# Kernel optimization log

Measured on AMD Instinct MI355X. Metric: run time of the kernel, lower is better.

Reference implementation:

```python
import jax, jax.numpy as jnp
import numpy as np

TOPK = 4


def setup_inputs() -> dict:
    key = jax.random.key(0)
    ks = jax.random.split(key, 9)
    B, T, D = 4, 2048, 1024
    E, H = 32, 128          # routed experts, per-expert hidden
    HS = H * TOPK           # shared expert hidden = 512
    s = lambda k, shape, fan: jax.random.normal(k, shape, dtype=jnp.float32) / np.sqrt(fan)
    return {
        "x": jax.random.normal(ks[0], (B, T, D), dtype=jnp.float32),
        "router_w": s(ks[1], (E, D), D),
        "router_bias": jnp.zeros((E,), dtype=jnp.float32),
        "gate_w": s(ks[2], (E, H, D), D),
        "up_w": s(ks[3], (E, H, D), D),
        "down_w": s(ks[4], (E, D, H), H),
        "sgate_w": s(ks[5], (HS, D), D),
        "sup_w": s(ks[6], (HS, D), D),
        "sdown_w": s(ks[7], (D, HS), HS),
    }


def reference(x, router_w, router_bias, gate_w, up_w, down_w, sgate_w, sup_w, sdown_w):
    B, T, D = x.shape
    flat = x.reshape(B * T, D)                                   # [N, D]
    # Router (fp32 logits + persistent bias buffer)
    logits = flat.astype(jnp.float32) @ router_w.T + router_bias  # [N, E]
    scores = jax.nn.softmax(logits, axis=-1)
    topk_scores, topk_idx = jax.lax.top_k(scores, TOPK)          # [N, K]
    topk_scores = topk_scores / jnp.clip(
        topk_scores.sum(axis=-1, keepdims=True), 1e-12, None)
    # Dense all-expert SwiGLU (matches torch.stack over experts)
    h = jax.nn.silu(jnp.einsum("nd,ehd->neh", flat, gate_w)) \
        * jnp.einsum("nd,ehd->neh", flat, up_w)                  # [N, E, H]
    expert_out = jnp.einsum("neh,edh->ned", h, down_w)           # [N, E, D]
    # Gather top-k expert outputs, scale, combine
    sel = jnp.take_along_axis(expert_out, topk_idx[:, :, None], axis=1)  # [N, K, D]
    out = (sel * topk_scores.astype(flat.dtype)[:, :, None]).sum(axis=1)  # [N, D]
    # Always-on shared expert (SwiGLU)
    out = out + (jax.nn.silu(flat @ sgate_w.T) * (flat @ sup_w.T)) @ sdown_w.T
    return out.reshape(B, T, D)
```

## Files before the change

### kernel.cpp

```cpp
#include <hip/hip_runtime.h>
#include <hip/hip_bf16.h>
#include <math.h>

#define N_TOK 8192
#define DIM   1024
#define E_R   32
#define H_E   128
#define HS    512
#define TOPK  4
#define RKS   8
#define RKL   (DIM / RKS)
#define MAXSLOT 34816

typedef __bf16 bf16;
typedef __bf16 bf16x8 __attribute__((ext_vector_type(8)));
typedef float  floatx4 __attribute__((ext_vector_type(4)));

#define MFMA16(a,b,c) __builtin_amdgcn_mfma_f32_16x16x32_bf16(a,b,c,0,0,0)

__device__ __forceinline__ void gl_lds16(const bf16* g, bf16* l) {
    __builtin_amdgcn_global_load_lds(
        (const __attribute__((address_space(1))) void*)g,
        (__attribute__((address_space(3))) void*)l, 16, 0, 0);
}

__global__ __launch_bounds__(256)
void cvt_all(const float* __restrict__ x, const float* __restrict__ g,
             const float* __restrict__ u, const float* __restrict__ d,
             const float* __restrict__ sg, const float* __restrict__ su,
             const float* __restrict__ sd,
             bf16* __restrict__ xb, bf16* __restrict__ gb, bf16* __restrict__ ub,
             bf16* __restrict__ db, bf16* __restrict__ sgb, bf16* __restrict__ sub,
             bf16* __restrict__ sdb) {
    int b = blockIdx.x;
    const float* s; bf16* o; int lb;
    if      (b < 4096)  { s = x;  o = xb;  lb = b; }
    else if (b < 6144)  { s = g;  o = gb;  lb = b - 4096; }
    else if (b < 8192)  { s = u;  o = ub;  lb = b - 6144; }
    else if (b < 10240) { s = d;  o = db;  lb = b - 8192; }
    else if (b < 10496) { s = sg; o = sgb; lb = b - 10240; }
    else if (b < 10752) { s = su; o = sub; lb = b - 10496; }
    else                { s = sd; o = sdb; lb = b - 10752; }
    size_t i = (size_t)lb * 2048 + threadIdx.x * 8;
    float4 v0 = *(const float4*)(s + i);
    float4 v1 = *(const float4*)(s + i + 4);
    bf16x8 r = {(bf16)v0.x,(bf16)v0.y,(bf16)v0.z,(bf16)v0.w,
                (bf16)v1.x,(bf16)v1.y,(bf16)v1.z,(bf16)v1.w};
    *(bf16x8*)(o + i) = r;
}

__global__ __launch_bounds__(256)
void router_gemm(const float* __restrict__ x, const float* __restrict__ rw,
                 float* __restrict__ partial) {
    __shared__ float Xs[64 * 132];
    __shared__ float Wt[128 * 32];
    int tid = threadIdx.x;
    int t0  = blockIdx.x * 64;
    int kb  = blockIdx.y * RKL;

#pragma unroll
    for (int j = 0; j < 8; ++j) {
        int flat = j * 1024 + tid * 4;
        int row = flat >> 7, col = flat & 127;
        float4 v = *(const float4*)(x + (size_t)(t0 + row) * DIM + kb + col);
        *(float4*)(&Xs[row * 132 + col]) = v;
    }
    {
        int e = tid >> 3, kq = (tid & 7) * 16;
        const float* wp = rw + (size_t)e * DIM + kb + kq;
#pragma unroll
        for (int i = 0; i < 16; i += 4) {
            float4 v = *(const float4*)(wp + i);
            Wt[(kq + i + 0) * 32 + e] = v.x;
            Wt[(kq + i + 1) * 32 + e] = v.y;
            Wt[(kq + i + 2) * 32 + e] = v.z;
            Wt[(kq + i + 3) * 32 + e] = v.w;
        }
    }
    __syncthreads();

    int eg = tid & 7, tg = tid >> 3;
    float acc[2][4] = {{0.f}};
#pragma unroll 4
    for (int k = 0; k < RKL; k += 4) {
        float4 xa0 = *(const float4*)(&Xs[(tg * 2 + 0) * 132 + k]);
        float4 xa1 = *(const float4*)(&Xs[(tg * 2 + 1) * 132 + k]);
#pragma unroll
        for (int kk = 0; kk < 4; ++kk) {
            float4 w = *(const float4*)(&Wt[(k + kk) * 32 + eg * 4]);
            float x0 = (&xa0.x)[kk], x1 = (&xa1.x)[kk];
            acc[0][0] += x0 * w.x; acc[0][1] += x0 * w.y;
            acc[0][2] += x0 * w.z; acc[0][3] += x0 * w.w;
            acc[1][0] += x1 * w.x; acc[1][1] += x1 * w.y;
            acc[1][2] += x1 * w.z; acc[1][3] += x1 * w.w;
        }
    }
#pragma unroll
    for (int t = 0; t < 2; ++t) {
        floatx4 v = { acc[t][0], acc[t][1], acc[t][2], acc[t][3] };
        *(floatx4*)(&partial[((size_t)blockIdx.y * N_TOK + t0 + tg * 2 + t) * 32 + eg * 4]) = v;
    }
}

__global__ __launch_bounds__(256)
void router_fin(const float* __restrict__ partial, const float* __restrict__ rb,
                int* __restrict__ counts, int* __restrict__ tlist,
                float* __restrict__ slist, int* __restrict__ tok2slot) {
    __shared__ int lcnt[E_R];
    __shared__ int gbase[E_R];
    int tid = threadIdx.x;
    int n = blockIdx.x * 256 + tid;
    if (tid < E_R) lcnt[tid] = 0;
    __syncthreads();

    float lg[E_R];
#pragma unroll
    for (int e4 = 0; e4 < E_R; e4 += 4) {
        floatx4 s = {0.f, 0.f, 0.f, 0.f};
#pragma unroll
        for (int ks = 0; ks < RKS; ++ks)
            s += *(const floatx4*)(&partial[((size_t)ks * N_TOK + n) * 32 + e4]);
        lg[e4 + 0] = s[0] + rb[e4 + 0];
        lg[e4 + 1] = s[1] + rb[e4 + 1];
        lg[e4 + 2] = s[2] + rb[e4 + 2];
        lg[e4 + 3] = s[3] + rb[e4 + 3];
    }
    float mx = -1e30f;
#pragma unroll
    for (int e = 0; e < E_R; ++e) mx = fmaxf(mx, lg[e]);
    float se = 0.f;
#pragma unroll
    for (int e = 0; e < E_R; ++e) { float v = __expf(lg[e] - mx); lg[e] = v; se += v; }
    float inv = 1.f / se;

    unsigned usedMask = 0;
    int idx[TOPK]; float pv[TOPK]; int lpos[TOPK]; float psum = 0.f;
    for (int k = 0; k < TOPK; ++k) {
        float best = -1.f; int bi = 0;
        for (int e = 0; e < E_R; ++e)
            if (!((usedMask >> e) & 1) && lg[e] > best) { best = lg[e]; bi = e; }
        usedMask |= 1u << bi;
        idx[k] = bi; pv[k] = best * inv; psum += pv[k];
    }
    float norm = 1.f / fmaxf(psum, 1e-12f);
#pragma unroll
    for (int k = 0; k < TOPK; ++k)
        lpos[k] = atomicAdd(&lcnt[idx[k]], 1);
    __syncthreads();
    if (tid < E_R) gbase[tid] = atomicAdd(&counts[tid], lcnt[tid]);
    __syncthreads();
#pragma unroll
    for (int k = 0; k < TOPK; ++k) {
        int e = idx[k];
        int pos = gbase[e] + lpos[k];
        tlist[(size_t)e * N_TOK + pos] = n;
        slist[(size_t)e * N_TOK + pos] = pv[k] * norm;
        tok2slot[(size_t)n * 4 + k] = (e << 16) | pos;
    }
}

__global__ void wq_build(const int* __restrict__ counts, int* __restrict__ items,
                         int* __restrict__ nitems, int* __restrict__ expbase) {
    if (threadIdx.x == 0) {
        int n = 0, base = 0;
        for (int e = 0; e < E_R; ++e) {
            int c = counts[e];
            expbase[e] = base;
            int nt = (c + 63) >> 6;
            for (int t = 0; t < nt; ++t)
                items[n++] = (e << 24) | (t << 16) | (base + t * 64);
            base += nt * 64;
        }
        *nitems = n;
    }
}

__global__ __launch_bounds__(256, 3)
void phase1(const bf16* __restrict__ xb, const bf16* __restrict__ wg,
            const bf16* __restrict__ wu, const bf16* __restrict__ sg,
            const bf16* __restrict__ su, const int* __restrict__ counts,
            const int* __restrict__ tlist, const int* __restrict__ items,
            const int* __restrict__ nitems,
            bf16* __restrict__ Hg, bf16* __restrict__ Hs) {
    __shared__ __align__(16) bf16 As[2 * 64 * 32];
    __shared__ __align__(16) bf16 Bs[2 * 256 * 32];

    int b = blockIdx.x;
    const bf16 *gptr, *uptr;
    bf16* hout; int hstride;
    int e, lbase, cnt = 0;
    if (b < 512) {
        int c = b >> 7, t = b & 127;
        gptr = sg + (size_t)c * H_E * DIM;
        uptr = su + (size_t)c * H_E * DIM;
        hout = Hs + (size_t)t * 64 * HS + c * H_E;
        hstride = HS;
        lbase = t * 64;
        e = -1;
    } else {
        int rbk = b - 512;
        if (rbk >= *nitems) return;
        int it = items[rbk];
        e = it >> 24; int t = (it >> 16) & 0xff; int rowbase = it & 0xffff;
        gptr = wg + (size_t)e * H_E * DIM;
        uptr = wu + (size_t)e * H_E * DIM;
        hout = Hg + (size_t)rowbase * H_E;
        hstride = H_E;
        cnt = counts[e];
        lbase = t * 64;
    }

    int tid = threadIdx.x;
    int r = tid >> 2;
    int chunk = (tid & 3) * 8;
    int tok;
    if (e < 0) tok = lbase + r;
    else { int li = lbase + r; if (li >= cnt) li = cnt - 1; tok = tlist[(size_t)e * N_TOK + li]; }
    const bf16* aSrc = xb + (size_t)tok * DIM + chunk;
    const bf16* gSrc = gptr + (size_t)r * DIM + chunk;
    const bf16* uSrc = uptr + (size_t)r * DIM + chunk;

    int w = tid >> 6, lane = tid & 63, m = lane & 15, quad = lane >> 4;

    floatx4 aG[4][2] = {{{0}}};
    floatx4 aU[4][2] = {{{0}}};

    #define P1_STAGE(buf, k0)                                                  \
        do {                                                                   \
            bf16* aD = As + (buf) * 2048 + tid * 8;                            \
            bf16* bD = Bs + (buf) * 8192 + tid * 8;                            \
            gl_lds16(aSrc + (k0), aD);                                         \
            gl_lds16(gSrc + (k0), bD);                                         \
            gl_lds16(gSrc + 64 * DIM + (k0), bD + 2048);                       \
            gl_lds16(uSrc + (k0), bD + 4096);                                  \
            gl_lds16(uSrc + 64 * DIM + (k0), bD + 6144);                       \
        } while (0)

    P1_STAGE(0, 0);
    __syncthreads();

    int cur = 0;
    for (int k0 = 0; k0 < DIM; k0 += 32) {
        if (k0 + 32 < DIM) P1_STAGE(cur ^ 1, k0 + 32);
        const bf16* Ab = As + cur * 2048;
        const bf16* Bb = Bs + cur * 8192;
        bf16x8 a[4], bg[2], bu[2];
#pragma unroll
        for (int mg = 0; mg < 4; ++mg)
            a[mg] = *(const bf16x8*)(Ab + (mg * 16 + m) * 32 + quad * 8);
#pragma unroll
        for (int j = 0; j < 2; ++j) {
            bg[j] = *(const bf16x8*)(Bb + (w * 32 + j * 16 + m) * 32 + quad * 8);
            bu[j] = *(const bf16x8*)(Bb + (128 + w * 32 + j * 16 + m) * 32 + quad * 8);
        }
#pragma unroll
        for (int j = 0; j < 2; ++j)
#pragma unroll
            for (int mg = 0; mg < 4; ++mg) {
                aG[mg][j] = MFMA16(a[mg], bg[j], aG[mg][j]);
                aU[mg][j] = MFMA16(a[mg], bu[j], aU[mg][j]);
            }
        __syncthreads();
        cur ^= 1;
    }
    #undef P1_STAGE

#pragma unroll
    for (int mg = 0; mg < 4; ++mg)
#pragma unroll
        for (int j = 0; j < 2; ++j)
#pragma unroll
            for (int r4 = 0; r4 < 4; ++r4) {
                float gv = aG[mg][j][r4], uv = aU[mg][j][r4];
                float h = gv / (1.f + __expf(-gv)) * uv;
                hout[(size_t)(mg * 16 + quad * 4 + r4) * hstride + w * 32 + j * 16 + m] = (bf16)h;
            }
}

__global__ __launch_bounds__(256, 3)
void phase2(const bf16* __restrict__ Hg, const bf16* __restrict__ wd,
            const int* __restrict__ counts, const float* __restrict__ slist,
            const int* __restrict__ items, const int* __restrict__ nitems,
            bf16* __restrict__ Od) {
    __shared__ __align__(16) bf16 As[2 * 64 * 32];
    __shared__ __align__(16) bf16 Bs[2 * 256 * 32];
    __shared__ float ssc[64];

    int rbk = blockIdx.x;
    if (rbk >= *nitems) return;
    int it = items[rbk];
    int e = it >> 24, t = (it >> 16) & 0xff, rowbase = it & 0xffff;
    int n0 = blockIdx.y * 256;
    int cnt = counts[e];

    int tid = threadIdx.x;
    if (tid < 64) {
        int li = t * 64 + tid;
        ssc[tid] = (li < cnt) ? slist[(size_t)e * N_TOK + li] : 0.f;
    }

    int r = tid >> 2, chunk = (tid & 3) * 8;
    const bf16* aSrc = Hg + (size_t)(rowbase + r) * H_E + chunk;
    const bf16* bSrc = wd + (size_t)e * DIM * H_E + (size_t)(n0 + r) * H_E + chunk;

    int w = tid >> 6, lane = tid & 63, m = lane & 15, quad = lane >> 4;
    floatx4 acc[4][4] = {{{0}}};

    #define P2_STAGE(buf, k0)                                                  \
        do {                                                                   \
            bf16* aD = As + (buf) * 2048 + tid * 8;                            \
            bf16* bD = Bs + (buf) * 8192 + tid * 8;                            \
            gl_lds16(aSrc + (k0), aD);                                         \
            _Pragma("unroll")                                                  \
            for (int p = 0; p < 4; ++p)                                        \
                gl_lds16(bSrc + (size_t)p * 64 * H_E + (k0), bD + p * 2048);   \
        } while (0)

    P2_STAGE(0, 0);
    __syncthreads();

    int cur = 0;
    for (int k0 = 0; k0 < H_E; k0 += 32) {
        if (k0 + 32 < H_E) P2_STAGE(cur ^ 1, k0 + 32);
        const bf16* Ab = As + cur * 2048;
        const bf16* Bb = Bs + cur * 8192;
        bf16x8 a[4], bb[4];
#pragma unroll
        for (int mg = 0; mg < 4; ++mg)
            a[mg] = *(const bf16x8*)(Ab + (mg * 16 + m) * 32 + quad * 8);
#pragma unroll
        for (int ng = 0; ng < 4; ++ng)
            bb[ng] = *(const bf16x8*)(Bb + (w * 64 + ng * 16 + m) * 32 + quad * 8);
#pragma unroll
        for (int ng = 0; ng < 4; ++ng)
#pragma unroll
            for (int mg = 0; mg < 4; ++mg)
                acc[mg][ng] = MFMA16(a[mg], bb[ng], acc[mg][ng]);
        __syncthreads();
        cur ^= 1;
    }
    #undef P2_STAGE

#pragma unroll
    for (int mg = 0; mg < 4; ++mg)
#pragma unroll
        for (int r4 = 0; r4 < 4; ++r4) {
            int row = mg * 16 + quad * 4 + r4;
            float sc = ssc[row];
            bf16* op = Od + (size_t)(rowbase + row) * DIM + n0 + w * 64 + m;
#pragma unroll
            for (int ng = 0; ng < 4; ++ng)
                op[ng * 16] = (bf16)(acc[mg][ng][r4] * sc);
        }
}

__global__ __launch_bounds__(256, 3)
void shared_down(const bf16* __restrict__ Hs, const bf16* __restrict__ sd,
                 const bf16* __restrict__ Od, const int* __restrict__ tok2slot,
                 const int* __restrict__ expbase, float* __restrict__ out) {
    __shared__ __align__(16) bf16 As[2 * 64 * 32];
    __shared__ __align__(16) bf16 Bs[2 * 256 * 32];
    __shared__ int srow[64][4];

    int t0 = blockIdx.x * 64;
    int n0 = blockIdx.y * 256;
    int tid = threadIdx.x;

    if (tid < 64) {
        const int* t2s = tok2slot + (size_t)(t0 + tid) * 4;
#pragma unroll
        for (int k = 0; k < 4; ++k) {
            int v = t2s[k];
            srow[tid][k] = expbase[v >> 16] + (v & 0xffff);
        }
    }

    int r = tid >> 2, chunk = (tid & 3) * 8;
    const bf16* aSrc = Hs + (size_t)(t0 + r) * HS + chunk;
    const bf16* bSrc = sd + (size_t)(n0 + r) * HS + chunk;

    int w = tid >> 6, lane = tid & 63, m = lane & 15, quad = lane >> 4;
    floatx4 acc[4][4] = {{{0}}};

    #define SD_STAGE(buf, k0)                                                  \
        do {                                                                   \
            bf16* aD = As + (buf) * 2048 + tid * 8;                            \
            bf16* bD = Bs + (buf) * 8192 + tid * 8;                            \
            gl_lds16(aSrc + (k0), aD);                                         \
            _Pragma("unroll")                                                  \
            for (int p = 0; p < 4; ++p)                                        \
                gl_lds16(bSrc + (size_t)p * 64 * HS + (k0), bD + p * 2048);    \
        } while (0)

    SD_STAGE(0, 0);
    __syncthreads();

    int cur = 0;
    for (int k0 = 0; k0 < HS; k0 += 32) {
        if (k0 + 32 < HS) SD_STAGE(cur ^ 1, k0 + 32);
        const bf16* Ab = As + cur * 2048;
        const bf16* Bb = Bs + cur * 8192;
        bf16x8 a[4], bb[4];
#pragma unroll
        for (int mg = 0; mg < 4; ++mg)
            a[mg] = *(const bf16x8*)(Ab + (mg * 16 + m) * 32 + quad * 8);
#pragma unroll
        for (int ng = 0; ng < 4; ++ng)
            bb[ng] = *(const bf16x8*)(Bb + (w * 64 + ng * 16 + m) * 32 + quad * 8);
#pragma unroll
        for (int ng = 0; ng < 4; ++ng)
#pragma unroll
            for (int mg = 0; mg < 4; ++mg)
                acc[mg][ng] = MFMA16(a[mg], bb[ng], acc[mg][ng]);
        __syncthreads();
        cur ^= 1;
    }
    #undef SD_STAGE

#pragma unroll
    for (int mg = 0; mg < 4; ++mg)
#pragma unroll
        for (int r4 = 0; r4 < 4; ++r4) {
            int rl = mg * 16 + quad * 4 + r4;
            size_t r0 = (size_t)srow[rl][0] * DIM;
            size_t r1 = (size_t)srow[rl][1] * DIM;
            size_t r2 = (size_t)srow[rl][2] * DIM;
            size_t r3 = (size_t)srow[rl][3] * DIM;
            float* op = out + (size_t)(t0 + rl) * DIM + n0 + w * 64 + m;
#pragma unroll
            for (int ng = 0; ng < 4; ++ng) {
                int col = n0 + w * 64 + ng * 16 + m;
                float v = acc[mg][ng][r4]
                        + (float)Od[r0 + col] + (float)Od[r1 + col]
                        + (float)Od[r2 + col] + (float)Od[r3 + col];
                op[ng * 16] = v;
            }
        }
}

extern "C" void kernel_launch(void* const* d_in, const int* in_sizes, int n_in,
                              void* d_out, int out_size, void* d_ws, size_t ws_size,
                              hipStream_t stream) {
    (void)in_sizes; (void)n_in; (void)out_size; (void)ws_size;
    const float* x   = (const float*)d_in[0];
    const float* rw  = (const float*)d_in[1];
    const float* rb  = (const float*)d_in[2];
    const float* gw  = (const float*)d_in[3];
    const float* uw  = (const float*)d_in[4];
    const float* dw  = (const float*)d_in[5];
    const float* sgw = (const float*)d_in[6];
    const float* suw = (const float*)d_in[7];
    const float* sdw = (const float*)d_in[8];
    float* out = (float*)d_out;

    char* ws = (char*)d_ws;
    size_t o = 0;
    bf16* xb  = (bf16*)(ws + o); o += (size_t)N_TOK * DIM * 2;
    bf16* wgb = (bf16*)(ws + o); o += (size_t)E_R * H_E * DIM * 2;
    bf16* wub = (bf16*)(ws + o); o += (size_t)E_R * H_E * DIM * 2;
    bf16* wdb = (bf16*)(ws + o); o += (size_t)E_R * DIM * H_E * 2;
    bf16* sgb = (bf16*)(ws + o); o += (size_t)HS * DIM * 2;
    bf16* sub = (bf16*)(ws + o); o += (size_t)HS * DIM * 2;
    bf16* sdb = (bf16*)(ws + o); o += (size_t)DIM * HS * 2;
    bf16* Hg  = (bf16*)(ws + o); o += (size_t)MAXSLOT * H_E * 2;
    bf16* Hs  = (bf16*)(ws + o); o += (size_t)N_TOK * HS * 2;
    bf16* Od  = (bf16*)(ws + o); o += (size_t)MAXSLOT * DIM * 2;
    float* partial = (float*)(ws + o); o += (size_t)RKS * N_TOK * 32 * 4;
    int*   counts = (int*)(ws + o);   o += 256;
    int*   tlist  = (int*)(ws + o);   o += (size_t)E_R * N_TOK * 4;
    float* slist  = (float*)(ws + o); o += (size_t)E_R * N_TOK * 4;
    int*   tok2slot = (int*)(ws + o); o += (size_t)N_TOK * 4 * 4;
    int*   items  = (int*)(ws + o);   o += 4096;
    int*   nitems = (int*)(ws + o);   o += 64;
    int*   expbase = (int*)(ws + o);  o += 256;

    hipMemsetAsync(counts, 0, E_R * sizeof(int), stream);

    router_gemm<<<dim3(N_TOK / 64, RKS), 256, 0, stream>>>(x, rw, partial);
    router_fin<<<N_TOK / 256, 256, 0, stream>>>(partial, rb, counts, tlist, slist,
                                                tok2slot);
    cvt_all<<<11008, 256, 0, stream>>>(x, gw, uw, dw, sgw, suw, sdw,
                                       xb, wgb, wub, wdb, sgb, sub, sdb);
    wq_build<<<1, 64, 0, stream>>>(counts, items, nitems, expbase);
    phase1<<<1056, 256, 0, stream>>>(xb, wgb, wub, sgb, sub, counts, tlist,
                                     items, nitems, Hg, Hs);
    phase2<<<dim3(544, 4), 256, 0, stream>>>(Hg, wdb, counts, slist,
                                             items, nitems, Od);
    shared_down<<<dim3(N_TOK / 64, 4), 256, 0, stream>>>(Hs, sdb, Od, tok2slot,
                                                         expbase, out);
}
```

Before: 307.9 us.

## Double K-tile depth to 64 with XOR-swizzled LDS layout in MoE GEMMs

All three GEMM kernels (phase1, phase2, shared_down) now stage 64-wide K slices instead of 32, which halves the number of barrier-separated iterations. The LDS tiles use an XOR swizzle on 16-byte chunks so that MFMA fragment reads avoid bank conflicts. The per-block shared-memory score and slot tables are replaced by direct global loads in the epilogues. Occupancy hints drop from 3 to 2 blocks per CU to fit the doubled LDS footprint, which trades some latency hiding for fewer syncs and wider loads.

```diff
diff --git a/kernel.cpp b/kernel.cpp
--- a/kernel.cpp
+++ b/kernel.cpp
@@ -175,15 +175,15 @@
     }
 }
 
-__global__ __launch_bounds__(256, 3)
+__global__ __launch_bounds__(256, 2)
 void phase1(const bf16* __restrict__ xb, const bf16* __restrict__ wg,
             const bf16* __restrict__ wu, const bf16* __restrict__ sg,
             const bf16* __restrict__ su, const int* __restrict__ counts,
             const int* __restrict__ tlist, const int* __restrict__ items,
             const int* __restrict__ nitems,
             bf16* __restrict__ Hg, bf16* __restrict__ Hs) {
-    __shared__ __align__(16) bf16 As[2 * 64 * 32];
-    __shared__ __align__(16) bf16 Bs[2 * 256 * 32];
+    __shared__ __align__(16) bf16 As[2 * 64 * 64];
+    __shared__ __align__(16) bf16 Bs[2 * 256 * 64];
 
     int b = blockIdx.x;
     const bf16 *gptr, *uptr;
@@ -211,55 +211,71 @@
     }
 
     int tid = threadIdx.x;
-    int r = tid >> 2;
-    int chunk = (tid & 3) * 8;
-    int tok;
-    if (e < 0) tok = lbase + r;
-    else { int li = lbase + r; if (li >= cnt) li = cnt - 1; tok = tlist[(size_t)e * N_TOK + li]; }
-    const bf16* aSrc = xb + (size_t)tok * DIM + chunk;
-    const bf16* gSrc = gptr + (size_t)r * DIM + chunk;
-    const bf16* uSrc = uptr + (size_t)r * DIM + chunk;
+    int rs = tid >> 3;
+    int cOff = ((tid & 7) ^ (rs & 7)) * 8;
+    int tokA, tokB;
+    if (e < 0) { tokA = lbase + rs; tokB = lbase + rs + 32; }
+    else {
+        int liA = lbase + rs;      if (liA >= cnt) liA = cnt - 1;
+        int liB = lbase + rs + 32; if (liB >= cnt) liB = cnt - 1;
+        tokA = tlist[(size_t)e * N_TOK + liA];
+        tokB = tlist[(size_t)e * N_TOK + liB];
+    }
+    const bf16* aSrc0 = xb + (size_t)tokA * DIM + cOff;
+    const bf16* aSrc1 = xb + (size_t)tokB * DIM + cOff;
+    const bf16* gSrc  = gptr + (size_t)rs * DIM + cOff;
+    const bf16* uSrc  = uptr + (size_t)rs * DIM + cOff;
 
     int w = tid >> 6, lane = tid & 63, m = lane & 15, quad = lane >> 4;
+    int mx7 = m & 7;
 
     floatx4 aG[4][2] = {{{0}}};
     floatx4 aU[4][2] = {{{0}}};
 
     #define P1_STAGE(buf, k0)                                                  \
         do {                                                                   \
-            bf16* aD = As + (buf) * 2048 + tid * 8;                            \
-            bf16* bD = Bs + (buf) * 8192 + tid * 8;                            \
-            gl_lds16(aSrc + (k0), aD);                                         \
-            gl_lds16(gSrc + (k0), bD);                                         \
-            gl_lds16(gSrc + 64 * DIM + (k0), bD + 2048);                       \
-            gl_lds16(uSrc + (k0), bD + 4096);                                  \
-            gl_lds16(uSrc + 64 * DIM + (k0), bD + 6144);                       \
+            bf16* aD = As + (buf) * 4096 + tid * 8;                            \
+            bf16* bD = Bs + (buf) * 16384 + tid * 8;                           \
+            gl_lds16(aSrc0 + (k0), aD);                                        \
+            gl_lds16(aSrc1 + (k0), aD + 2048);                                 \
+            gl_lds16(gSrc + (k0),            bD);                              \
+            gl_lds16(gSrc + 32 * DIM + (k0), bD + 2048);                       \
+            gl_lds16(gSrc + 64 * DIM + (k0), bD + 4096);                       \
+            gl_lds16(gSrc + 96 * DIM + (k0), bD + 6144);                       \
+            gl_lds16(uSrc + (k0),            bD + 8192);                       \
+            gl_lds16(uSrc + 32 * DIM + (k0), bD + 10240);                      \
+            gl_lds16(uSrc + 64 * DIM + (k0), bD + 12288);                      \
+            gl_lds16(uSrc + 96 * DIM + (k0), bD + 14336);                      \
         } while (0)
 
     P1_STAGE(0, 0);
     __syncthreads();
 
     int cur = 0;
-    for (int k0 = 0; k0 < DIM; k0 += 32) {
-        if (k0 + 32 < DIM) P1_STAGE(cur ^ 1, k0 + 32);
-        const bf16* Ab = As + cur * 2048;
-        const bf16* Bb = Bs + cur * 8192;
-        bf16x8 a[4], bg[2], bu[2];
-#pragma unroll
-        for (int mg = 0; mg < 4; ++mg)
-            a[mg] = *(const bf16x8*)(Ab + (mg * 16 + m) * 32 + quad * 8);
-#pragma unroll
-        for (int j = 0; j < 2; ++j) {
-            bg[j] = *(const bf16x8*)(Bb + (w * 32 + j * 16 + m) * 32 + quad * 8);
-            bu[j] = *(const bf16x8*)(Bb + (128 + w * 32 + j * 16 + m) * 32 + quad * 8);
-        }
-#pragma unroll
-        for (int j = 0; j < 2; ++j)
-#pragma unroll
-            for (int mg = 0; mg < 4; ++mg) {
-                aG[mg][j] = MFMA16(a[mg], bg[j], aG[mg][j]);
-                aU[mg][j] = MFMA16(a[mg], bu[j], aU[mg][j]);
+    for (int k0 = 0; k0 < DIM; k0 += 64) {
+        if (k0 + 64 < DIM) P1_STAGE(cur ^ 1, k0 + 64);
+        const bf16* Ab = As + cur * 4096;
+        const bf16* Bb = Bs + cur * 16384;
+#pragma unroll
+        for (int kh = 0; kh < 2; ++kh) {
+            int cx = ((kh * 4 + quad) ^ mx7) * 8;
+            bf16x8 a[4], bg[2], bu[2];
+#pragma unroll
+            for (int mg = 0; mg < 4; ++mg)
+                a[mg] = *(const bf16x8*)(Ab + (mg * 16 + m) * 64 + cx);
+#pragma unroll
+            for (int j = 0; j < 2; ++j) {
+                bg[j] = *(const bf16x8*)(Bb + (w * 32 + j * 16 + m) * 64 + cx);
+                bu[j] = *(const bf16x8*)(Bb + (128 + w * 32 + j * 16 + m) * 64 + cx);
             }
+#pragma unroll
+            for (int j = 0; j < 2; ++j)
+#pragma unroll
+                for (int mg = 0; mg < 4; ++mg) {
+                    aG[mg][j] = MFMA16(a[mg], bg[j], aG[mg][j]);
+                    aU[mg][j] = MFMA16(a[mg], bu[j], aU[mg][j]);
+                }
+        }
         __syncthreads();
         cur ^= 1;
     }
@@ -277,14 +293,13 @@
             }
 }
 
-__global__ __launch_bounds__(256, 3)
+__global__ __launch_bounds__(256, 2)
 void phase2(const bf16* __restrict__ Hg, const bf16* __restrict__ wd,
             const int* __restrict__ counts, const float* __restrict__ slist,
             const int* __restrict__ items, const int* __restrict__ nitems,
             bf16* __restrict__ Od) {
-    __shared__ __align__(16) bf16 As[2 * 64 * 32];
-    __shared__ __align__(16) bf16 Bs[2 * 256 * 32];
-    __shared__ float ssc[64];
+    __shared__ __align__(16) bf16 As[2 * 64 * 64];
+    __shared__ __align__(16) bf16 Bs[2 * 256 * 64];
 
     int rbk = blockIdx.x;
     if (rbk >= *nitems) return;
@@ -294,48 +309,51 @@
     int cnt = counts[e];
 
     int tid = threadIdx.x;
-    if (tid < 64) {
-        int li = t * 64 + tid;
-        ssc[tid] = (li < cnt) ? slist[(size_t)e * N_TOK + li] : 0.f;
-    }
-
-    int r = tid >> 2, chunk = (tid & 3) * 8;
-    const bf16* aSrc = Hg + (size_t)(rowbase + r) * H_E + chunk;
-    const bf16* bSrc = wd + (size_t)e * DIM * H_E + (size_t)(n0 + r) * H_E + chunk;
+    int rs = tid >> 3;
+    int cOff = ((tid & 7) ^ (rs & 7)) * 8;
+    const bf16* aSrc0 = Hg + (size_t)(rowbase + rs) * H_E + cOff;
+    const bf16* aSrc1 = Hg + (size_t)(rowbase + rs + 32) * H_E + cOff;
+    const bf16* bSrc  = wd + (size_t)e * DIM * H_E + (size_t)(n0 + rs) * H_E + cOff;
 
     int w = tid >> 6, lane = tid & 63, m = lane & 15, quad = lane >> 4;
+    int mx7 = m & 7;
     floatx4 acc[4][4] = {{{0}}};
 
     #define P2_STAGE(buf, k0)                                                  \
         do {                                                                   \
-            bf16* aD = As + (buf) * 2048 + tid * 8;                            \
-            bf16* bD = Bs + (buf) * 8192 + tid * 8;                            \
-            gl_lds16(aSrc + (k0), aD);                                         \
+            bf16* aD = As + (buf) * 4096 + tid * 8;                            \
+            bf16* bD = Bs + (buf) * 16384 + tid * 8;                           \
+            gl_lds16(aSrc0 + (k0), aD);                                        \
+            gl_lds16(aSrc1 + (k0), aD + 2048);                                 \
             _Pragma("unroll")                                                  \
-            for (int p = 0; p < 4; ++p)                                        \
-                gl_lds16(bSrc + (size_t)p * 64 * H_E + (k0), bD + p * 2048);   \
+            for (int p = 0; p < 8; ++p)                                        \
+                gl_lds16(bSrc + (size_t)p * 32 * H_E + (k0), bD + p * 2048);   \
         } while (0)
 
     P2_STAGE(0, 0);
     __syncthreads();
 
     int cur = 0;
-    for (int k0 = 0; k0 < H_E; k0 += 32) {
-        if (k0 + 32 < H_E) P2_STAGE(cur ^ 1, k0 + 32);
-        const bf16* Ab = As + cur * 2048;
-        const bf16* Bb = Bs + cur * 8192;
-        bf16x8 a[4], bb[4];
-#pragma unroll
-        for (int mg = 0; mg < 4; ++mg)
-            a[mg] = *(const bf16x8*)(Ab + (mg * 16 + m) * 32 + quad * 8);
-#pragma unroll
-        for (int ng = 0; ng < 4; ++ng)
-            bb[ng] = *(const bf16x8*)(Bb + (w * 64 + ng * 16 + m) * 32 + quad * 8);
-#pragma unroll
-        for (int ng = 0; ng < 4; ++ng)
+    for (int k0 = 0; k0 < H_E; k0 += 64) {
+        if (k0 + 64 < H_E) P2_STAGE(cur ^ 1, k0 + 64);
+        const bf16* Ab = As + cur * 4096;
+        const bf16* Bb = Bs + cur * 16384;
+#pragma unroll
+        for (int kh = 0; kh < 2; ++kh) {
+            int cx = ((kh * 4 + quad) ^ mx7) * 8;
+            bf16x8 a[4], bb[4];
 #pragma unroll
             for (int mg = 0; mg < 4; ++mg)
-                acc[mg][ng] = MFMA16(a[mg], bb[ng], acc[mg][ng]);
+                a[mg] = *(const bf16x8*)(Ab + (mg * 16 + m) * 64 + cx);
+#pragma unroll
+            for (int ng = 0; ng < 4; ++ng)
+                bb[ng] = *(const bf16x8*)(Bb + (w * 64 + ng * 16 + m) * 64 + cx);
+#pragma unroll
+            for (int ng = 0; ng < 4; ++ng)
+#pragma unroll
+                for (int mg = 0; mg < 4; ++mg)
+                    acc[mg][ng] = MFMA16(a[mg], bb[ng], acc[mg][ng]);
+        }
         __syncthreads();
         cur ^= 1;
     }
@@ -346,7 +364,8 @@
 #pragma unroll
         for (int r4 = 0; r4 < 4; ++r4) {
             int row = mg * 16 + quad * 4 + r4;
-            float sc = ssc[row];
+            int li = t * 64 + row;
+            float sc = (li < cnt) ? slist[(size_t)e * N_TOK + li] : 0.f;
             bf16* op = Od + (size_t)(rowbase + row) * DIM + n0 + w * 64 + m;
 #pragma unroll
             for (int ng = 0; ng < 4; ++ng)
@@ -354,64 +373,62 @@
         }
 }
 
-__global__ __launch_bounds__(256, 3)
+__global__ __launch_bounds__(256, 2)
 void shared_down(const bf16* __restrict__ Hs, const bf16* __restrict__ sd,
                  const bf16* __restrict__ Od, const int* __restrict__ tok2slot,
                  const int* __restrict__ expbase, float* __restrict__ out) {
-    __shared__ __align__(16) bf16 As[2 * 64 * 32];
-    __shared__ __align__(16) bf16 Bs[2 * 256 * 32];
-    __shared__ int srow[64][4];
+    __shared__ __align__(16) bf16 As[2 * 64 * 64];
+    __shared__ __align__(16) bf16 Bs[2 * 256 * 64];
 
     int t0 = blockIdx.x * 64;
     int n0 = blockIdx.y * 256;
     int tid = threadIdx.x;
 
-    if (tid < 64) {
-        const int* t2s = tok2slot + (size_t)(t0 + tid) * 4;
-#pragma unroll
-        for (int k = 0; k < 4; ++k) {
-            int v = t2s[k];
-            srow[tid][k] = expbase[v >> 16] + (v & 0xffff);
-        }
-    }
-
-    int r = tid >> 2, chunk = (tid & 3) * 8;
-    const bf16* aSrc = Hs + (size_t)(t0 + r) * HS + chunk;
-    const bf16* bSrc = sd + (size_t)(n0 + r) * HS + chunk;
+    int rs = tid >> 3;
+    int cOff = ((tid & 7) ^ (rs & 7)) * 8;
+    const bf16* aSrc0 = Hs + (size_t)(t0 + rs) * HS + cOff;
+    const bf16* aSrc1 = Hs + (size_t)(t0 + rs + 32) * HS + cOff;
+    const bf16* bSrc  = sd + (size_t)(n0 + rs) * HS + cOff;
 
     int w = tid >> 6, lane = tid & 63, m = lane & 15, quad = lane >> 4;
+    int mx7 = m & 7;
     floatx4 acc[4][4] = {{{0}}};
 
     #define SD_STAGE(buf, k0)                                                  \
         do {                                                                   \
-            bf16* aD = As + (buf) * 2048 + tid * 8;                            \
-            bf16* bD = Bs + (buf) * 8192 + tid * 8;                            \
-            gl_lds16(aSrc + (k0), aD);                                         \
+            bf16* aD = As + (buf) * 4096 + tid * 8;                            \
+            bf16* bD = Bs + (buf) * 16384 + tid * 8;                           \
+            gl_lds16(aSrc0 + (k0), aD);                                        \
+            gl_lds16(aSrc1 + (k0), aD + 2048);                                 \
             _Pragma("unroll")                                                  \
-            for (int p = 0; p < 4; ++p)                                        \
-                gl_lds16(bSrc + (size_t)p * 64 * HS + (k0), bD + p * 2048);    \
+            for (int p = 0; p < 8; ++p)                                        \
+                gl_lds16(bSrc + (size_t)p * 32 * HS + (k0), bD + p * 2048);    \
         } while (0)
 
     SD_STAGE(0, 0);
     __syncthreads();
 
     int cur = 0;
-    for (int k0 = 0; k0 < HS; k0 += 32) {
-        if (k0 + 32 < HS) SD_STAGE(cur ^ 1, k0 + 32);
-        const bf16* Ab = As + cur * 2048;
-        const bf16* Bb = Bs + cur * 8192;
-        bf16x8 a[4], bb[4];
-#pragma unroll
-        for (int mg = 0; mg < 4; ++mg)
-            a[mg] = *(const bf16x8*)(Ab + (mg * 16 + m) * 32 + quad * 8);
-#pragma unroll
-        for (int ng = 0; ng < 4; ++ng)
-            bb[ng] = *(const bf16x8*)(Bb + (w * 64 + ng * 16 + m) * 32 + quad * 8);
-#pragma unroll
-        for (int ng = 0; ng < 4; ++ng)
+    for (int tt = 0; tt < 8; ++tt) {
+        if (tt < 7) SD_STAGE(cur ^ 1, (tt + 1) * 64);
+        const bf16* Ab = As + cur * 4096;
+        const bf16* Bb = Bs + cur * 16384;
+#pragma unroll
+        for (int kh = 0; kh < 2; ++kh) {
+            int cx = ((kh * 4 + quad) ^ mx7) * 8;
+            bf16x8 a[4], bb[4];
 #pragma unroll
             for (int mg = 0; mg < 4; ++mg)
-                acc[mg][ng] = MFMA16(a[mg], bb[ng], acc[mg][ng]);
+                a[mg] = *(const bf16x8*)(Ab + (mg * 16 + m) * 64 + cx);
+#pragma unroll
+            for (int ng = 0; ng < 4; ++ng)
+                bb[ng] = *(const bf16x8*)(Bb + (w * 64 + ng * 16 + m) * 64 + cx);
+#pragma unroll
+            for (int ng = 0; ng < 4; ++ng)
+#pragma unroll
+                for (int mg = 0; mg < 4; ++mg)
+                    acc[mg][ng] = MFMA16(a[mg], bb[ng], acc[mg][ng]);
+        }
         __syncthreads();
         cur ^= 1;
     }
@@ -422,10 +439,12 @@
 #pragma unroll
         for (int r4 = 0; r4 < 4; ++r4) {
             int rl = mg * 16 + quad * 4 + r4;
-            size_t r0 = (size_t)srow[rl][0] * DIM;
-            size_t r1 = (size_t)srow[rl][1] * DIM;
-            size_t r2 = (size_t)srow[rl][2] * DIM;
-            size_t r3 = (size_t)srow[rl][3] * DIM;
+            const int* t2s = tok2slot + (size_t)(t0 + rl) * 4;
+            int v0 = t2s[0], v1 = t2s[1], v2 = t2s[2], v3 = t2s[3];
+            size_t r0 = (size_t)(expbase[v0 >> 16] + (v0 & 0xffff)) * DIM;
+            size_t r1 = (size_t)(expbase[v1 >> 16] + (v1 & 0xffff)) * DIM;
+            size_t r2 = (size_t)(expbase[v2 >> 16] + (v2 & 0xffff)) * DIM;
+            size_t r3 = (size_t)(expbase[v3 >> 16] + (v3 & 0xffff)) * DIM;
             float* op = out + (size_t)(t0 + rl) * DIM + n0 + w * 64 + m;
 #pragma unroll
             for (int ng = 0; ng < 4; ++ng) {
```

Result: no change. 311.4 us (+1.1%).
